# Optimization experiments

Measured on AMD Instinct MI355X. Metric: run time of the kernel, lower is better.

The kernel has to match this reference:

```python
import jax, jax.numpy as jnp
import numpy as np

B, T, C = 2, 2048, 1024
H = 16
DH = C // H  # 64
DFF = 4 * C  # 4096
EPS = 1e-5


def layernorm(x, gamma, beta):
    # torch.var defaults to unbiased (ddof=1) -- replicate exactly
    m = jnp.mean(x, axis=-1, keepdims=True)
    v = jnp.var(x, axis=-1, ddof=1, keepdims=True)
    return (x - m) / jnp.sqrt(v + EPS) * gamma + beta


def setup_inputs() -> dict:
    key = jax.random.key(0)
    ks = jax.random.split(key, 12)
    s = 0.02
    return {
        "x": jax.random.normal(ks[0], (B, T, C), jnp.float32),
        "Wq": jax.random.normal(ks[1], (H, C, DH), jnp.float32) * s,
        "bq": jnp.zeros((H, DH), jnp.float32),
        "Wk": jax.random.normal(ks[2], (H, C, DH), jnp.float32) * s,
        "bk": jnp.zeros((H, DH), jnp.float32),
        "Wv": jax.random.normal(ks[3], (H, C, DH), jnp.float32) * s,
        "bv": jnp.zeros((H, DH), jnp.float32),
        "Wo": jax.random.normal(ks[4], (C, C), jnp.float32) * s,
        "bo": jnp.zeros((C,), jnp.float32),
        "gamma1": jnp.ones((C,), jnp.float32),
        "beta1": jnp.zeros((C,), jnp.float32),
        "gamma2": jnp.ones((C,), jnp.float32),
        "beta2": jnp.zeros((C,), jnp.float32),
        "W1": jax.random.normal(ks[5], (C, DFF), jnp.float32) * s,
        "b1": jnp.zeros((DFF,), jnp.float32),
        "W2": jax.random.normal(ks[6], (DFF, C), jnp.float32) * s,
        "b2": jnp.zeros((C,), jnp.float32),
    }


def reference(x, Wq, bq, Wk, bk, Wv, bv, Wo, bo,
              gamma1, beta1, gamma2, beta2, W1, b1, W2, b2):
    Tn = x.shape[1]
    # Block: x = ln1(x); x = x + attn(x); x = ln2(x); out = x + ffw(x)
    x = layernorm(x, gamma1, beta1)

    # per-head Q/K/V linears, stacked over heads: [B,T,C] x [H,C,Dh] -> [B,H,T,Dh]
    q = jnp.einsum('btc,hcd->bhtd', x, Wq) + bq[None, :, None, :]
    k = jnp.einsum('btc,hcd->bhtd', x, Wk) + bk[None, :, None, :]
    v = jnp.einsum('btc,hcd->bhtd', x, Wv) + bv[None, :, None, :]

    scale = DH ** -0.5
    scores = jnp.einsum('bhtd,bhsd->bhts', q, k) * scale  # [B,H,T,T]
    causal = jnp.tril(jnp.ones((Tn, Tn), dtype=bool))
    scores = jnp.where(causal, scores, -jnp.inf)
    alpha = jax.nn.softmax(scores, axis=-1)
    h = jnp.einsum('bhts,bhsd->bhtd', alpha, v)  # [B,H,T,Dh]
    h = jnp.transpose(h, (0, 2, 1, 3)).reshape(x.shape)  # concat heads -> [B,T,C]
    attn_out = h @ Wo + bo

    x = x + attn_out
    x = layernorm(x, gamma2, beta2)
    ffw = jax.nn.gelu(x @ W1 + b1, approximate=False) @ W2 + b2
    return x + ffw
```

## Files before the change

kernel.cpp:

```cpp
#include <hip/hip_runtime.h>

typedef unsigned short u16;
typedef unsigned int u32;
typedef __attribute__((ext_vector_type(8))) short bf16x8;
typedef __attribute__((ext_vector_type(4))) float f32x4;

#define AS1 __attribute__((address_space(1)))
#define AS3 __attribute__((address_space(3)))

__device__ __forceinline__ u16 f2bf(float f) {
  u32 u = __float_as_uint(f);
  u = (u + 0x7fffu + ((u >> 16) & 1u)) >> 16;
  return (u16)u;
}
__device__ __forceinline__ float bf2f(u16 v) { return __uint_as_float((u32)v << 16); }

__device__ __forceinline__ void gl16(const void* g, void* l) {
  __builtin_amdgcn_global_load_lds((AS1 void*)g, (AS3 void*)l, 16, 0, 0);
}

__device__ __forceinline__ float exp2a(float x) {
  float r;
  asm("v_exp_f32 %0, %1" : "=v"(r) : "v"(x));
  return r;
}
__device__ __forceinline__ u32 pk2(float lo, float hi) {
  u32 r;
  asm("v_cvt_pk_bf16_f32 %0, %1, %2" : "=v"(r) : "v"(lo), "v"(hi));
  return r;
}

#define LGKM0()                                         \
  do {                                                  \
    asm volatile("s_waitcnt lgkmcnt(0)" ::: "memory");  \
    __builtin_amdgcn_sched_barrier(0);                  \
  } while (0)
#define VMC0()                                          \
  do {                                                  \
    asm volatile("s_waitcnt vmcnt(0)" ::: "memory");    \
    __builtin_amdgcn_sched_barrier(0);                  \
  } while (0)

__global__ __launch_bounds__(256) void wprep_kernel(
    const float* __restrict__ Wq, const float* __restrict__ Wk,
    const float* __restrict__ Wv, const float* __restrict__ Wo,
    const float* __restrict__ W1, const float* __restrict__ W2,
    u16* __restrict__ WqkvT, u16* __restrict__ WoT,
    u16* __restrict__ W1T, u16* __restrict__ W2T,
    const float* __restrict__ x, const float* __restrict__ gamma,
    const float* __restrict__ beta, u16* __restrict__ xn_bf) {
  __shared__ float tile[32][33];
  __shared__ float rs[4], rq[4];
  int id = blockIdx.x;
  const int tx = threadIdx.x, ty = threadIdx.y;
  if (id >= 12288) {
    const int row = id - 12288;
    const int tid = ty * 32 + tx;
    const float* xr = x + (long)row * 1024;
    float4 v = *(const float4*)(xr + tid * 4);
    float s = v.x + v.y + v.z + v.w;
    float sq = v.x * v.x + v.y * v.y + v.z * v.z + v.w * v.w;
#pragma unroll
    for (int off = 1; off < 64; off <<= 1) {
      s += __shfl_xor(s, off);
      sq += __shfl_xor(sq, off);
    }
    const int w = tid >> 6, lane = tid & 63;
    if (lane == 0) { rs[w] = s; rq[w] = sq; }
    __syncthreads();
    s = rs[0] + rs[1] + rs[2] + rs[3];
    sq = rq[0] + rq[1] + rq[2] + rq[3];
    const float mean = s * (1.0f / 1024.0f);
    const float var = (sq - 1024.0f * mean * mean) * (1.0f / 1023.0f);
    const float rstd = rsqrtf(var + 1e-5f);
    float4 g4 = *(const float4*)(gamma + tid * 4);
    float4 b4 = *(const float4*)(beta + tid * 4);
    ushort4 ub;
    ub.x = f2bf((v.x - mean) * rstd * g4.x + b4.x);
    ub.y = f2bf((v.y - mean) * rstd * g4.y + b4.y);
    ub.z = f2bf((v.z - mean) * rstd * g4.z + b4.z);
    ub.w = f2bf((v.w - mean) * rstd * g4.w + b4.w);
    *(ushort4*)(xn_bf + (long)row * 1024 + tid * 4) = ub;
    return;
  }
  const float* ip;
  u16* op;
  int in_rs, R, c0, r0;
  if (id < 3072) {
    const int xq = id & 1, y = (id >> 1) & 31, z = id >> 6;
    const float* in = z < 16 ? Wq : (z < 32 ? Wk : Wv);
    ip = in + (long)(z & 15) * 65536;
    op = WqkvT + (long)z * 65536;
    in_rs = 64; R = 1024; c0 = xq * 32; r0 = y * 32;
  } else if (id < 4096) {
    id -= 3072;
    ip = Wo; op = WoT; in_rs = 1024; R = 1024;
    c0 = (id & 31) * 32; r0 = (id >> 5) * 32;
  } else if (id < 8192) {
    id -= 4096;
    ip = W1; op = W1T; in_rs = 4096; R = 1024;
    c0 = (id & 127) * 32; r0 = (id >> 7) * 32;
  } else {
    id -= 8192;
    ip = W2; op = W2T; in_rs = 1024; R = 4096;
    c0 = (id & 31) * 32; r0 = (id >> 5) * 32;
  }
#pragma unroll
  for (int i = 0; i < 4; ++i)
    tile[ty + i * 8][tx] = ip[(long)(r0 + ty + i * 8) * in_rs + c0 + tx];
  __syncthreads();
#pragma unroll
  for (int i = 0; i < 4; ++i)
    op[(long)(c0 + ty + i * 8) * R + r0 + tx] = f2bf(tile[tx][ty + i * 8]);
}

__global__ __launch_bounds__(256) void ln2_fused_kernel(
    const u16* __restrict__ p0, const u16* __restrict__ p1,
    const float* __restrict__ bo, const u16* __restrict__ xnbf,
    const float* __restrict__ gamma, const float* __restrict__ beta,
    u16* __restrict__ obf) {
  const int row = blockIdx.x;
  const int tid = threadIdx.x;
  const long i4 = (long)row * 1024 + tid * 4;
  ushort4 a0 = *(const ushort4*)(p0 + i4);
  ushort4 a1 = *(const ushort4*)(p1 + i4);
  ushort4 xv = *(const ushort4*)(xnbf + i4);
  float4 bv = *(const float4*)(bo + tid * 4);
  float y0 = bf2f(a0.x) + bf2f(a1.x) + bv.x + bf2f(xv.x);
  float y1 = bf2f(a0.y) + bf2f(a1.y) + bv.y + bf2f(xv.y);
  float y2 = bf2f(a0.z) + bf2f(a1.z) + bv.z + bf2f(xv.z);
  float y3 = bf2f(a0.w) + bf2f(a1.w) + bv.w + bf2f(xv.w);
  float s = y0 + y1 + y2 + y3;
  float sq = y0 * y0 + y1 * y1 + y2 * y2 + y3 * y3;
#pragma unroll
  for (int off = 1; off < 64; off <<= 1) {
    s += __shfl_xor(s, off);
    sq += __shfl_xor(sq, off);
  }
  __shared__ float rs[4], rq[4];
  const int w = tid >> 6, lane = tid & 63;
  if (lane == 0) { rs[w] = s; rq[w] = sq; }
  __syncthreads();
  s = rs[0] + rs[1] + rs[2] + rs[3];
  sq = rq[0] + rq[1] + rq[2] + rq[3];
  const float mean = s * (1.0f / 1024.0f);
  const float var = (sq - 1024.0f * mean * mean) * (1.0f / 1023.0f);
  const float rstd = rsqrtf(var + 1e-5f);
  float4 g4 = *(const float4*)(gamma + tid * 4);
  float4 b4 = *(const float4*)(beta + tid * 4);
  ushort4 ub;
  ub.x = f2bf((y0 - mean) * rstd * g4.x + b4.x);
  ub.y = f2bf((y1 - mean) * rstd * g4.y + b4.y);
  ub.z = f2bf((y2 - mean) * rstd * g4.z + b4.z);
  ub.w = f2bf((y3 - mean) * rstd * g4.w + b4.w);
  *(ushort4*)(obf + i4) = ub;
}

__global__ __launch_bounds__(256) void ffn2_reduce_kernel(const u16* __restrict__ p,
                                                          const float* __restrict__ b2,
                                                          const u16* __restrict__ ynbf,
                                                          float* __restrict__ out) {
  const long i4 = ((long)blockIdx.x * 256 + threadIdx.x) * 4;
  ushort4 p0 = *(const ushort4*)(p + i4);
  ushort4 p1 = *(const ushort4*)(p + 4194304 + i4);
  ushort4 rr = *(const ushort4*)(ynbf + i4);
  const int nn = (int)(i4 & 1023);
  float4 bb = *(const float4*)(b2 + nn);
  float4 o;
  o.x = bf2f(p0.x) + bf2f(p1.x) + bb.x + bf2f(rr.x);
  o.y = bf2f(p0.y) + bf2f(p1.y) + bb.y + bf2f(rr.y);
  o.z = bf2f(p0.z) + bf2f(p1.z) + bb.z + bf2f(rr.z);
  o.w = bf2f(p0.w) + bf2f(p1.w) + bb.w + bf2f(rr.w);
  *(float4*)(out + i4) = o;
}

template <int EPI>
__global__ __launch_bounds__(256, 2) void gemm128_kernel(
    const u16* __restrict__ A, const u16* __restrict__ Bt,
    int K, int nk, int N,
    const float* bias0, const float* bias1, const float* bias2,
    void* out0, void* out1) {
  __shared__ __align__(16) u16 Asm[128 * 64];
  __shared__ __align__(16) u16 Bsm[128 * 64];
  const int tid = threadIdx.x;
  const int lane = tid & 63, w = tid >> 6;
  const int wm = w >> 1, wn = w & 1;
  const int q = lane & 15, g = lane >> 4;
  const long m0 = (long)blockIdx.x * 128;
  const long n0 = (long)blockIdx.y * 128;
  const int bz = blockIdx.z;
  const long koff = (long)bz * (long)nk * 64;

  f32x4 zero4 = {0.f, 0.f, 0.f, 0.f};
  f32x4 acc[4][4];
#pragma unroll
  for (int mi = 0; mi < 4; ++mi)
#pragma unroll
    for (int ni = 0; ni < 4; ++ni) acc[mi][ni] = zero4;

  for (int ks = 0; ks < nk; ++ks) {
    __syncthreads();
    const u16* ga = A + m0 * K + koff + ks * 64;
    const u16* gb = Bt + n0 * K + koff + ks * 64;
    const int base = w * 256;
#pragma unroll
    for (int i = 0; i < 4; ++i) {
      const int idx = base + i * 64 + lane;
      const int row = idx >> 3;
      const int lg = (idx & 7) ^ (row & 7);
      gl16(ga + (long)row * K + lg * 8, Asm + (long)(base + i * 64) * 8);
    }
#pragma unroll
    for (int i = 0; i < 4; ++i) {
      const int idx = base + i * 64 + lane;
      const int row = idx >> 3;
      const int lg = (idx & 7) ^ (row & 7);
      gl16(gb + (long)row * K + lg * 8, Bsm + (long)(base + i * 64) * 8);
    }
    __syncthreads();
#pragma unroll
    for (int half = 0; half < 2; ++half) {
      bf16x8 af[4], bfv[4];
#pragma unroll
      for (int mi = 0; mi < 4; ++mi) {
        const int row = wm * 64 + mi * 16 + q;
        const int ph = (half * 4 + g) ^ (row & 7);
        af[mi] = *(const bf16x8*)(Asm + row * 64 + ph * 8);
      }
#pragma unroll
      for (int ni = 0; ni < 4; ++ni) {
        const int row = wn * 64 + ni * 16 + q;
        const int ph = (half * 4 + g) ^ (row & 7);
        bfv[ni] = *(const bf16x8*)(Bsm + row * 64 + ph * 8);
      }
#pragma unroll
      for (int mi = 0; mi < 4; ++mi)
#pragma unroll
        for (int ni = 0; ni < 4; ++ni)
          acc[mi][ni] = __builtin_amdgcn_mfma_f32_16x16x32_bf16(af[mi], bfv[ni],
                                                                acc[mi][ni], 0, 0, 0);
    }
  }
#pragma unroll
  for (int mi = 0; mi < 4; ++mi) {
#pragma unroll
    for (int ni = 0; ni < 4; ++ni) {
      const long mbase = m0 + wm * 64 + mi * 16 + 4 * g;
      const long n = n0 + wn * 64 + ni * 16 + q;
      f32x4 a = acc[mi][ni];
      if constexpr (EPI == 0) {
        const int sel = (int)(n >> 10);
        const int nn = (int)(n & 1023);
        const float* bp = sel == 0 ? bias0 : (sel == 1 ? bias1 : bias2);
        const float bb2 = bp[nn];
        if (sel < 2) {
          const float sc = (sel == 0) ? 0.18033688011112043f : 1.0f;
          u16* qkp = (u16*)out0;
#pragma unroll
          for (int r = 0; r < 4; ++r)
            qkp[(mbase + r) * 2048 + n] = f2bf((a[r] + bb2) * sc);
        } else {
          const int bI = (int)(mbase >> 11);
          const int t = (int)(mbase & 2047);
          const int hh = nn >> 6, dh = nn & 63;
          ushort4 pk;
          pk.x = f2bf(a[0] + bb2); pk.y = f2bf(a[1] + bb2);
          pk.z = f2bf(a[2] + bb2); pk.w = f2bf(a[3] + bb2);
          *(ushort4*)((u16*)out1 + ((long)((bI * 16 + hh) * 64 + dh)) * 2048 + t) = pk;
        }
      } else if constexpr (EPI == 2) {
        u16* gp = (u16*)out0;
        const float bb2 = bias0[(int)n];
#pragma unroll
        for (int r = 0; r < 4; ++r) {
          const float xg = a[r] + bb2;
          const float ge = 0.5f * xg * (1.0f + erff(xg * 0.70710678118f));
          gp[(mbase + r) * N + n] = f2bf(ge);
        }
      } else {
        u16* pp = (u16*)out0 + (long)bz * 4096 * 1024;
#pragma unroll
        for (int r = 0; r < 4; ++r) pp[(mbase + r) * 1024 + n] = f2bf(a[r]);
      }
    }
  }
}

__device__ __forceinline__ void attn_stage(const u16* kbase, const u16* vtb, int kb,
                                           u16* Kd, u16* Vd, int tid) {
#pragma unroll
  for (int it = 0; it < 2; ++it) {
    const int gi = it * 256 + tid;
    const int row = gi >> 3;
    const int lg = (gi & 7) ^ (row & 7);
    gl16(kbase + (long)(kb * 64 + row) * 2048 + lg * 8, Kd + gi * 8);
    gl16(vtb + (long)row * 2048 + kb * 64 + lg * 8, Vd + gi * 8);
  }
}

__device__ __forceinline__ void softmax_slab(const f32x4 st[4], bool diag, int qrow,
                                             int kb, int g, int q15,
                                             float& m2, float& l, u16* prow,
                                             float al[4]) {
  float sv[4][4];
  float rmax = -1e30f;
#pragma unroll
  for (int sub = 0; sub < 4; ++sub)
#pragma unroll
    for (int r = 0; r < 4; ++r) {
      float s_ = st[sub][r];
      if (diag) {
        const int key = kb * 64 + sub * 16 + 4 * g + r;
        s_ = (key > qrow) ? -1e30f : s_;
      }
      sv[sub][r] = s_;
      rmax = fmaxf(rmax, s_);
    }
  rmax = fmaxf(rmax, __shfl_xor(rmax, 16));
  rmax = fmaxf(rmax, __shfl_xor(rmax, 32));
  const float mnew = fmaxf(m2, rmax);
  const float alpha = exp2a(m2 - mnew);
  float psum = 0.f;
#pragma unroll
  for (int sub = 0; sub < 4; ++sub) {
    const float p0 = exp2a(sv[sub][0] - mnew);
    const float p1 = exp2a(sv[sub][1] - mnew);
    const float p2 = exp2a(sv[sub][2] - mnew);
    const float p3 = exp2a(sv[sub][3] - mnew);
    uint2 u;
    u.x = pk2(p0, p1);
    u.y = pk2(p2, p3);
    *(uint2*)(prow + sub * 16 + 4 * g) = u;
    psum += (p0 + p1) + (p2 + p3);
  }
  psum += __shfl_xor(psum, 16);
  psum += __shfl_xor(psum, 32);
  l = l * alpha + psum;
  m2 = mnew;
#pragma unroll
  for (int r = 0; r < 4; ++r) al[r] = __shfl(alpha, 4 * g + r);
}

__global__ __launch_bounds__(256, 2) void attn_kernel(const u16* __restrict__ qk,
                                                      const u16* __restrict__ vT,
                                                      u16* __restrict__ o) {
  __shared__ __align__(16) u16 Ksm[2][64 * 64];
  __shared__ __align__(16) u16 Vsm[2][64 * 64];
  __shared__ __align__(16) u16 Psm[8][16][72];
  const int lid = blockIdx.x;
  const int xcd = lid & 7, s6 = lid >> 3;
  const int b2 = (s6 >> 4) & 3, xr = s6 & 15;
  const int qs = (b2 & 2) ? (15 - xr) : xr;
  const int bh = xcd + 8 * b2;
  const int b = bh >> 4, h = bh & 15;
  const int tid = threadIdx.x, lane = tid & 63, w = tid >> 6;
  const int q15 = lane & 15, g = lane >> 4;
  const u16* qbase = qk + (long)b * 2048 * 2048 + h * 64;
  const u16* kbase = qbase + 1024;
  const u16* vtb = vT + (long)bh * 64 * 2048;
  f32x4 zero4 = {0.f, 0.f, 0.f, 0.f};

  const int r0 = qs * 128 + w * 16 + q15;
  bf16x8 qa[2][2];
  qa[0][0] = *(const bf16x8*)(qbase + (long)r0 * 2048 + g * 8);
  qa[0][1] = *(const bf16x8*)(qbase + (long)r0 * 2048 + 32 + g * 8);
  qa[1][0] = *(const bf16x8*)(qbase + (long)(r0 + 64) * 2048 + g * 8);
  qa[1][1] = *(const bf16x8*)(qbase + (long)(r0 + 64) * 2048 + 32 + g * 8);

  f32x4 oa0[4], oa1[4];
#pragma unroll
  for (int dv = 0; dv < 4; ++dv) { oa0[dv] = zero4; oa1[dv] = zero4; }
  float m20 = -1e30f, l0 = 0.f, m21 = -1e30f, l1 = 0.f;
  const int kbmax = 2 * qs + 1;

  attn_stage(kbase, vtb, 0, Ksm[0], Vsm[0], tid);
  VMC0();
  __syncthreads();

  for (int kb = 0; kb <= kbmax; ++kb) {
    const int buf = kb & 1;
    if (kb < kbmax) attn_stage(kbase, vtb, kb + 1, Ksm[buf ^ 1], Vsm[buf ^ 1], tid);
    const u16* Kb = Ksm[buf];
    const u16* Vb = Vsm[buf];
    const bool s0on = (kb <= 2 * qs);
    f32x4 st0[4], st1[4];
#pragma unroll
    for (int sub = 0; sub < 4; ++sub) {
      const int row = sub * 16 + q15;
      const bf16x8 ka0 = *(const bf16x8*)(Kb + row * 64 + ((g ^ (row & 7)) * 8));
      const bf16x8 ka1 = *(const bf16x8*)(Kb + row * 64 + (((4 + g) ^ (row & 7)) * 8));
      f32x4 z = zero4;
      z = __builtin_amdgcn_mfma_f32_16x16x32_bf16(ka0, qa[1][0], z, 0, 0, 0);
      z = __builtin_amdgcn_mfma_f32_16x16x32_bf16(ka1, qa[1][1], z, 0, 0, 0);
      st1[sub] = z;
      if (s0on) {
        f32x4 z0 = zero4;
        z0 = __builtin_amdgcn_mfma_f32_16x16x32_bf16(ka0, qa[0][0], z0, 0, 0, 0);
        z0 = __builtin_amdgcn_mfma_f32_16x16x32_bf16(ka1, qa[0][1], z0, 0, 0, 0);
        st0[sub] = z0;
      }
    }
    float al0[4], al1[4];
    if (s0on)
      softmax_slab(st0, kb == 2 * qs, r0, kb, g, q15, m20, l0, &Psm[w * 2][q15][0], al0);
    softmax_slab(st1, kb == 2 * qs + 1, r0 + 64, kb, g, q15, m21, l1,
                 &Psm[w * 2 + 1][q15][0], al1);
    if (s0on)
#pragma unroll
      for (int dv = 0; dv < 4; ++dv) {
        oa0[dv][0] *= al0[0]; oa0[dv][1] *= al0[1];
        oa0[dv][2] *= al0[2]; oa0[dv][3] *= al0[3];
      }
#pragma unroll
    for (int dv = 0; dv < 4; ++dv) {
      oa1[dv][0] *= al1[0]; oa1[dv][1] *= al1[1];
      oa1[dv][2] *= al1[2]; oa1[dv][3] *= al1[3];
    }
    LGKM0();
#pragma unroll
    for (int half = 0; half < 2; ++half) {
      const bf16x8 pa0 = *(const bf16x8*)(&Psm[w * 2][q15][half * 32 + 8 * g]);
      const bf16x8 pa1 = *(const bf16x8*)(&Psm[w * 2 + 1][q15][half * 32 + 8 * g]);
#pragma unroll
      for (int dv = 0; dv < 4; ++dv) {
        const int row = dv * 16 + q15;
        const bf16x8 vb = *(const bf16x8*)(Vb + row * 64 + (((half * 4 + g) ^ (row & 7)) * 8));
        if (s0on) oa0[dv] = __builtin_amdgcn_mfma_f32_16x16x32_bf16(pa0, vb, oa0[dv], 0, 0, 0);
        oa1[dv] = __builtin_amdgcn_mfma_f32_16x16x32_bf16(pa1, vb, oa1[dv], 0, 0, 0);
      }
    }
    VMC0();
    __syncthreads();
  }
  const float li0 = 1.0f / l0, li1 = 1.0f / l1;
  float v0[4], v1[4];
#pragma unroll
  for (int r = 0; r < 4; ++r) {
    v0[r] = __shfl(li0, 4 * g + r);
    v1[r] = __shfl(li1, 4 * g + r);
  }
  const int tok0 = b * 2048 + qs * 128 + w * 16;
#pragma unroll
  for (int dv = 0; dv < 4; ++dv)
#pragma unroll
    for (int r = 0; r < 4; ++r) {
      o[(long)(tok0 + 4 * g + r) * 1024 + h * 64 + dv * 16 + q15] =
          f2bf(oa0[dv][r] * v0[r]);
      o[(long)(tok0 + 64 + 4 * g + r) * 1024 + h * 64 + dv * 16 + q15] =
          f2bf(oa1[dv][r] * v1[r]);
    }
}

extern "C" void kernel_launch(void* const* d_in, const int* in_sizes, int n_in,
                              void* d_out, int out_size, void* d_ws, size_t ws_size,
                              hipStream_t stream) {
  (void)in_sizes; (void)n_in; (void)out_size; (void)ws_size;
  const float* x  = (const float*)d_in[0];
  const float* Wq = (const float*)d_in[1];
  const float* bq = (const float*)d_in[2];
  const float* Wk = (const float*)d_in[3];
  const float* bk = (const float*)d_in[4];
  const float* Wv = (const float*)d_in[5];
  const float* bv = (const float*)d_in[6];
  const float* Wo = (const float*)d_in[7];
  const float* bo = (const float*)d_in[8];
  const float* g1 = (const float*)d_in[9];
  const float* be1 = (const float*)d_in[10];
  const float* g2 = (const float*)d_in[11];
  const float* be2 = (const float*)d_in[12];
  const float* W1 = (const float*)d_in[13];
  const float* b1 = (const float*)d_in[14];
  const float* W2 = (const float*)d_in[15];
  const float* b2 = (const float*)d_in[16];

  char* ws = (char*)d_ws;
  u16*   xn_bf = (u16*)  (ws + 0);
  u16*   WqkvT = (u16*)  (ws + 25165824);
  u16*   WoT   = (u16*)  (ws + 31457280);
  u16*   W1T   = (u16*)  (ws + 33554432);
  u16*   W2T   = (u16*)  (ws + 41943040);
  u16*   qkb   = (u16*)  (ws + 50331648);
  u16*   vTb   = (u16*)  (ws + 67108864);
  u16*   ah    = (u16*)  (ws + 75497472);
  u16*   pwo0  = (u16*)  (ws + 50331648);
  u16*   gbuf  = (u16*)  (ws + 50331648);
  u16*   part  = (u16*)  (ws + 8388608);
  u16*   yn_bf = (u16*)  (ws + 83886080);

  dim3 tb(32, 8), b256(256);
  wprep_kernel<<<dim3(16384), tb, 0, stream>>>(Wq, Wk, Wv, Wo, W1, W2,
                                               WqkvT, WoT, W1T, W2T,
                                               x, g1, be1, xn_bf);
  gemm128_kernel<0><<<dim3(32, 24, 1), b256, 0, stream>>>(xn_bf, WqkvT, 1024, 16, 3072,
                                                          bq, bk, bv, qkb, vTb);
  attn_kernel<<<dim3(512), b256, 0, stream>>>(qkb, vTb, ah);
  gemm128_kernel<5><<<dim3(32, 8, 2), b256, 0, stream>>>(ah, WoT, 1024, 8, 1024,
                                                         nullptr, nullptr, nullptr, pwo0, nullptr);
  ln2_fused_kernel<<<dim3(4096), b256, 0, stream>>>(pwo0, pwo0 + 4194304, bo, xn_bf,
                                                    g2, be2, yn_bf);
  gemm128_kernel<2><<<dim3(32, 32, 1), b256, 0, stream>>>(yn_bf, W1T, 1024, 16, 4096,
                                                          b1, nullptr, nullptr, gbuf, nullptr);
  gemm128_kernel<5><<<dim3(32, 8, 2), b256, 0, stream>>>(gbuf, W2T, 4096, 32, 1024,
                                                         nullptr, nullptr, nullptr, part, nullptr);
  ffn2_reduce_kernel<<<dim3(4096), b256, 0, stream>>>(part, b2, yn_bf, (float*)d_out);
}
```

Measured before the change: 208.8 us.

## Software-pipeline attention: triple-buffer K/V and overlap next QK with softmax/PV

The attention loop is unrolled by two and uses three shared-memory K/V buffers. The QK^T MFMAs for the next key block are issued before the softmax and PV of the current block, so matrix work can hide softmax latency and LDS waits. Two blocks are prefetched up front. The per-row-slab causal skip (s0on) is gone: the first slab is computed on the final diagonal block and then masked, which adds some wasted MFMAs, more registers and more LDS use.

```diff
diff --git a/kernel.cpp b/kernel.cpp
--- a/kernel.cpp
+++ b/kernel.cpp
@@ -341,11 +341,55 @@
   for (int r = 0; r < 4; ++r) al[r] = __shfl(alpha, 4 * g + r);
 }
 
+#define MFMA_ __builtin_amdgcn_mfma_f32_16x16x32_bf16
+
+#define QKCOMP(D0, D1, Kb)                                                     \
+  do {                                                                         \
+    _Pragma("unroll") for (int sub = 0; sub < 4; ++sub) {                      \
+      const int row = sub * 16 + q15;                                          \
+      const bf16x8 ka0 = *(const bf16x8*)((Kb) + row * 64 + ((g ^ (row & 7)) * 8)); \
+      const bf16x8 ka1 = *(const bf16x8*)((Kb) + row * 64 + (((4 + g) ^ (row & 7)) * 8)); \
+      f32x4 z0 = zero4, z1 = zero4;                                            \
+      z0 = MFMA_(ka0, qa[0][0], z0, 0, 0, 0);                                  \
+      z0 = MFMA_(ka1, qa[0][1], z0, 0, 0, 0);                                  \
+      D0[sub] = z0;                                                            \
+      z1 = MFMA_(ka0, qa[1][0], z1, 0, 0, 0);                                  \
+      z1 = MFMA_(ka1, qa[1][1], z1, 0, 0, 0);                                  \
+      D1[sub] = z1;                                                            \
+    }                                                                          \
+  } while (0)
+
+#define SMPV(S0, S1, KB, Vb)                                                   \
+  do {                                                                         \
+    float al0[4], al1[4];                                                      \
+    softmax_slab(S0, (KB) >= 2 * qs, r0, (KB), g, q15, m20, l0,                \
+                 &Psm[w * 2][q15][0], al0);                                    \
+    softmax_slab(S1, (KB) == 2 * qs + 1, r0 + 64, (KB), g, q15, m21, l1,       \
+                 &Psm[w * 2 + 1][q15][0], al1);                                \
+    _Pragma("unroll") for (int dv = 0; dv < 4; ++dv) {                         \
+      oa0[dv][0] *= al0[0]; oa0[dv][1] *= al0[1];                              \
+      oa0[dv][2] *= al0[2]; oa0[dv][3] *= al0[3];                              \
+      oa1[dv][0] *= al1[0]; oa1[dv][1] *= al1[1];                              \
+      oa1[dv][2] *= al1[2]; oa1[dv][3] *= al1[3];                              \
+    }                                                                          \
+    LGKM0();                                                                   \
+    _Pragma("unroll") for (int half = 0; half < 2; ++half) {                   \
+      const bf16x8 pa0 = *(const bf16x8*)(&Psm[w * 2][q15][half * 32 + 8 * g]); \
+      const bf16x8 pa1 = *(const bf16x8*)(&Psm[w * 2 + 1][q15][half * 32 + 8 * g]); \
+      _Pragma("unroll") for (int dv = 0; dv < 4; ++dv) {                       \
+        const int row = dv * 16 + q15;                                         \
+        const bf16x8 vb = *(const bf16x8*)((Vb) + row * 64 + (((half * 4 + g) ^ (row & 7)) * 8)); \
+        oa0[dv] = MFMA_(pa0, vb, oa0[dv], 0, 0, 0);                            \
+        oa1[dv] = MFMA_(pa1, vb, oa1[dv], 0, 0, 0);                            \
+      }                                                                        \
+    }                                                                          \
+  } while (0)
+
 __global__ __launch_bounds__(256, 2) void attn_kernel(const u16* __restrict__ qk,
                                                       const u16* __restrict__ vT,
                                                       u16* __restrict__ o) {
-  __shared__ __align__(16) u16 Ksm[2][64 * 64];
-  __shared__ __align__(16) u16 Vsm[2][64 * 64];
+  __shared__ __align__(16) u16 Ksm[3][4096];
+  __shared__ __align__(16) u16 Vsm[3][4096];
   __shared__ __align__(16) u16 Psm[8][16][72];
   const int lid = blockIdx.x;
   const int xcd = lid & 7, s6 = lid >> 3;
@@ -374,64 +418,28 @@
   const int kbmax = 2 * qs + 1;
 
   attn_stage(kbase, vtb, 0, Ksm[0], Vsm[0], tid);
-  VMC0();
+  attn_stage(kbase, vtb, 1, Ksm[1], Vsm[1], tid);
+  asm volatile("s_waitcnt vmcnt(4)" ::: "memory");
+  __builtin_amdgcn_sched_barrier(0);
   __syncthreads();
-
-  for (int kb = 0; kb <= kbmax; ++kb) {
-    const int buf = kb & 1;
-    if (kb < kbmax) attn_stage(kbase, vtb, kb + 1, Ksm[buf ^ 1], Vsm[buf ^ 1], tid);
-    const u16* Kb = Ksm[buf];
-    const u16* Vb = Vsm[buf];
-    const bool s0on = (kb <= 2 * qs);
-    f32x4 st0[4], st1[4];
-#pragma unroll
-    for (int sub = 0; sub < 4; ++sub) {
-      const int row = sub * 16 + q15;
-      const bf16x8 ka0 = *(const bf16x8*)(Kb + row * 64 + ((g ^ (row & 7)) * 8));
-      const bf16x8 ka1 = *(const bf16x8*)(Kb + row * 64 + (((4 + g) ^ (row & 7)) * 8));
-      f32x4 z = zero4;
-      z = __builtin_amdgcn_mfma_f32_16x16x32_bf16(ka0, qa[1][0], z, 0, 0, 0);
-      z = __builtin_amdgcn_mfma_f32_16x16x32_bf16(ka1, qa[1][1], z, 0, 0, 0);
-      st1[sub] = z;
-      if (s0on) {
-        f32x4 z0 = zero4;
-        z0 = __builtin_amdgcn_mfma_f32_16x16x32_bf16(ka0, qa[0][0], z0, 0, 0, 0);
-        z0 = __builtin_amdgcn_mfma_f32_16x16x32_bf16(ka1, qa[0][1], z0, 0, 0, 0);
-        st0[sub] = z0;
-      }
-    }
-    float al0[4], al1[4];
-    if (s0on)
-      softmax_slab(st0, kb == 2 * qs, r0, kb, g, q15, m20, l0, &Psm[w * 2][q15][0], al0);
-    softmax_slab(st1, kb == 2 * qs + 1, r0 + 64, kb, g, q15, m21, l1,
-                 &Psm[w * 2 + 1][q15][0], al1);
-    if (s0on)
-#pragma unroll
-      for (int dv = 0; dv < 4; ++dv) {
-        oa0[dv][0] *= al0[0]; oa0[dv][1] *= al0[1];
-        oa0[dv][2] *= al0[2]; oa0[dv][3] *= al0[3];
-      }
-#pragma unroll
-    for (int dv = 0; dv < 4; ++dv) {
-      oa1[dv][0] *= al1[0]; oa1[dv][1] *= al1[1];
-      oa1[dv][2] *= al1[2]; oa1[dv][3] *= al1[3];
-    }
-    LGKM0();
-#pragma unroll
-    for (int half = 0; half < 2; ++half) {
-      const bf16x8 pa0 = *(const bf16x8*)(&Psm[w * 2][q15][half * 32 + 8 * g]);
-      const bf16x8 pa1 = *(const bf16x8*)(&Psm[w * 2 + 1][q15][half * 32 + 8 * g]);
-#pragma unroll
-      for (int dv = 0; dv < 4; ++dv) {
-        const int row = dv * 16 + q15;
-        const bf16x8 vb = *(const bf16x8*)(Vb + row * 64 + (((half * 4 + g) ^ (row & 7)) * 8));
-        if (s0on) oa0[dv] = __builtin_amdgcn_mfma_f32_16x16x32_bf16(pa0, vb, oa0[dv], 0, 0, 0);
-        oa1[dv] = __builtin_amdgcn_mfma_f32_16x16x32_bf16(pa1, vb, oa1[dv], 0, 0, 0);
-      }
-    }
+  f32x4 sA0[4], sA1[4], sB0[4], sB1[4];
+  QKCOMP(sA0, sA1, Ksm[0]);
+
+  for (int t = 0; t <= kbmax; t += 2) {
     VMC0();
     __syncthreads();
-  }
+    if (t + 2 <= kbmax)
+      attn_stage(kbase, vtb, t + 2, Ksm[(t + 2) % 3], Vsm[(t + 2) % 3], tid);
+    QKCOMP(sB0, sB1, Ksm[(t + 1) % 3]);
+    SMPV(sA0, sA1, t, Vsm[t % 3]);
+    VMC0();
+    __syncthreads();
+    if (t + 3 <= kbmax)
+      attn_stage(kbase, vtb, t + 3, Ksm[(t + 3) % 3], Vsm[(t + 3) % 3], tid);
+    if (t + 2 <= kbmax) QKCOMP(sA0, sA1, Ksm[(t + 2) % 3]);
+    SMPV(sB0, sB1, t + 1, Vsm[(t + 1) % 3]);
+  }
+
   const float li0 = 1.0f / l0, li1 = 1.0f / l1;
   float v0[4], v1[4];
 #pragma unroll
```

Result: slower. 216.7 us (+3.8%).
